# Kernel tuning notes

Hardware: AMD Instinct MI355X
Metric: run time of the kernel (lower is better)

Reference implementation:

```python
import jax, jax.numpy as jnp
import numpy as np

B, S, D = 1, 4096, 2048
M = 4                  # compression rate
NC = S // M            # compressed slots
TOPK = 512
NH, C = 16, 64         # query heads, head dim
DC = 512               # query compression dim
NG, DG = 4, 512        # output projection groups, intermediate dim
CI, NHI = 64, 4        # indexer head dim, indexer heads
ROPE = 32              # partial rope dims (last ROPE of C)
EPS = 1e-6
NEG = -1e30


def _ln(x, w, b):
    mu = x.mean(-1, keepdims=True)
    var = ((x - mu) ** 2).mean(-1, keepdims=True)
    return (x - mu) * jax.lax.rsqrt(var + EPS) * w + b


def _rope(q, pos):
    # partial RoPE on the last ROPE dims of q [B,S,NH,C]; keys are NOT rotated (faithful)
    x_part, x_rope = q[..., :C - ROPE], q[..., C - ROPE:]
    x0, x1 = x_rope[..., 0::2], x_rope[..., 1::2]
    inv = 1.0 / (10000.0 ** (jnp.arange(0, ROPE, 2, dtype=jnp.float32) / ROPE))
    ang = pos[:, None].astype(jnp.float32) * inv[None]           # [S, ROPE/2]
    cos = jnp.cos(ang)[None, :, None, :]
    sin = jnp.sin(ang)[None, :, None, :]
    r = x0 * cos - x1 * sin
    i = x0 * sin + x1 * cos
    rot = jnp.stack([r, i], -1).reshape(x_rope.shape)
    return jnp.concatenate([x_part, rot], -1)


def reference(x, w_kv_a, w_kv_b, w_z_a, w_z_b, b_a, b_b, w_dq, w_iuq, w_w, w_k,
              w_uq, o_down, o_up, kvn_w, kvn_b, qn_w, qn_b, sink_logits):
    pos = jnp.arange(S)
    # ---- token-level compressor: windowed (2m-wide, m-stride) per-channel softmax ----
    c_a = (x @ w_kv_a).reshape(B, NC, M, C)
    c_b = (x @ w_kv_b).reshape(B, NC, M, C)
    z_a = (x @ w_z_a).reshape(B, NC, M, C)
    z_b = (x @ w_z_b).reshape(B, NC, M, C)
    prev_z = jnp.concatenate([jnp.full((B, 1, M, C), NEG, x.dtype), z_b[:, :-1]], 1)
    prev_c = jnp.concatenate([jnp.zeros((B, 1, M, C), x.dtype), c_b[:, :-1]], 1)
    logits = jnp.concatenate([prev_z + b_b, z_a + b_a], 2)        # [B,NC,2M,C]
    wts = jax.nn.softmax(logits, axis=2)
    compressed = (wts * jnp.concatenate([prev_c, c_a], 2)).sum(2)  # [B,NC,C]
    # ---- lightning indexer: relu multi-head scores + causal mask + top-k ----
    c_q = x @ w_dq                                                 # [B,S,DC]
    q_i = (c_q @ w_iuq).reshape(B, S, NHI, CI)
    hw = x @ w_w                                                   # [B,S,NHI]
    k_orig = x.reshape(B, NC, M, D).mean(2)
    k_proj = k_orig @ w_k                                          # [B,NC,CI]
    dot = jnp.einsum('bshc,bkc->bskh', q_i, k_proj)
    iscores = (jax.nn.relu(dot) * hw[:, :, None, :]).sum(-1)       # [B,S,NC]
    imask = jnp.arange(NC)[None, None, :] < pos[None, :, None]     # NC//S + 1 == 1
    iscores = jnp.where(imask, iscores, -jnp.inf)
    _, top_idx = jax.lax.top_k(iscores, TOPK)                      # [B,S,K]
    # ---- sparse attention over gathered compressed KV ----
    q = (c_q @ w_uq).reshape(B, S, NH, C)
    kc = _ln(compressed, kvn_w, kvn_b)
    q = _rope(_ln(q, qn_w, qn_b), pos)
    k_sel = kc[jnp.arange(B)[:, None, None], top_idx]              # [B,S,K,C]
    scores = jnp.einsum('bshc,bskc->bhsk', q, k_sel) / jnp.sqrt(jnp.float32(C))
    cmask = pos[None, None, :, None] < (top_idx[:, None, :, :] * M)
    scores = jnp.where(cmask, scores, -jnp.inf)
    e = jnp.exp(scores)
    denom = e.sum(-1, keepdims=True) + jnp.exp(sink_logits)[None, :, None, None]
    attn = e / denom                                               # sink-augmented softmax
    out = jnp.einsum('bhsk,bskc->bshc', attn, k_sel).reshape(B, S, NH * C)
    g = jnp.einsum('bsgd,gde->bsge', out.reshape(B, S, NG, (NH * C) // NG), o_down)
    return g.reshape(B, S, NG * DG) @ o_up


def setup_inputs() -> dict:
    key = jax.random.key(0)
    ks = jax.random.split(key, 20)
    lin = lambda k, fi, fo: jax.random.normal(k, (fi, fo), jnp.float32) / np.sqrt(fi)
    return {
        'x': jax.random.normal(ks[0], (B, S, D), jnp.float32),
        'w_kv_a': lin(ks[1], D, C), 'w_kv_b': lin(ks[2], D, C),
        'w_z_a': lin(ks[3], D, C), 'w_z_b': lin(ks[4], D, C),
        'b_a': 0.02 * jax.random.normal(ks[5], (M, C), jnp.float32),
        'b_b': 0.02 * jax.random.normal(ks[6], (M, C), jnp.float32),
        'w_dq': lin(ks[7], D, DC),
        'w_iuq': lin(ks[8], DC, CI * NHI),
        'w_w': lin(ks[9], D, NHI),
        'w_k': lin(ks[10], D, CI),
        'w_uq': lin(ks[11], DC, NH * C),
        'o_down': jax.random.normal(ks[12], (NG, (NH * C) // NG, DG), jnp.float32) / np.sqrt((NH * C) // NG),
        'o_up': lin(ks[13], NG * DG, D),
        'kvn_w': 1.0 + 0.02 * jax.random.normal(ks[14], (C,), jnp.float32),
        'kvn_b': 0.02 * jax.random.normal(ks[15], (C,), jnp.float32),
        'qn_w': 1.0 + 0.02 * jax.random.normal(ks[16], (C,), jnp.float32),
        'qn_b': 0.02 * jax.random.normal(ks[17], (C,), jnp.float32),
        'sink_logits': 0.02 * jax.random.normal(ks[18], (NH,), jnp.float32),
    }
```

## Files before the change

kernel.cpp:

```cpp
#include <hip/hip_runtime.h>
#include <math.h>

#define S_   4096
#define D_   2048
#define M_   4
#define NC_  1024
#define TOPK_ 512
#define NH_  16
#define C_   64
#define DC_  512
#define NG_  4
#define DG_  512
#define CI_  64
#define NHI_ 4
#define ROPE_ 32
#define EPS_ 1e-6f

typedef __attribute__((ext_vector_type(8))) short short8;
typedef __attribute__((ext_vector_type(4))) short short4v;
typedef __attribute__((ext_vector_type(4))) float floatx4;

__device__ inline unsigned short f2bf(float f) {
  unsigned u = __float_as_uint(f);
  u += 0x7fff + ((u >> 16) & 1);
  return (unsigned short)(u >> 16);
}
__device__ inline float bf2f(unsigned short h) {
  return __uint_as_float(((unsigned)h) << 16);
}

__global__ __launch_bounds__(256) void gemm_bf16_64(
    const unsigned short* __restrict__ A, const unsigned short* __restrict__ Bt,
    float* __restrict__ Cf, unsigned short* __restrict__ Cb,
    int K, int lda, int ldb, int ldc,
    long long Az, long long Bz, long long Cz) {
  int zz = blockIdx.z;
  A += (size_t)zz * Az;
  Bt += (size_t)zz * Bz;
  if (Cf) Cf += (size_t)zz * Cz;
  if (Cb) Cb += (size_t)zz * Cz;
  __shared__ unsigned short As[64 * 32];
  __shared__ unsigned short Bs[128 * 32];
  int tid = threadIdx.x;
  int bm = blockIdx.y * 64, bn = blockIdx.x * 128;
  int lane = tid & 63, wid = tid >> 6;
  int wm = (wid & 1) * 32, wn = (wid >> 1) * 64;
  int qd = lane >> 4, m16 = lane & 15;

  floatx4 acc[2][4];
#pragma unroll
  for (int i = 0; i < 2; ++i)
#pragma unroll
    for (int j = 0; j < 4; ++j) acc[i][j] = (floatx4){0.f, 0.f, 0.f, 0.f};

  for (int k0 = 0; k0 < K; k0 += 32) {
    {
      int r = tid >> 2, sl = tid & 3;
      int g = sl ^ ((r >> 1) & 3);
      __builtin_amdgcn_global_load_lds(
          (const __attribute__((address_space(1))) unsigned int*)(A + (size_t)(bm + r) * lda + k0 + g * 8),
          (__attribute__((address_space(3))) unsigned int*)(&As[tid * 8]), 16, 0, 0);
    }
#pragma unroll
    for (int i = 0; i < 2; ++i) {
      int idx = tid + 256 * i;
      int r = idx >> 2, sl = idx & 3;
      int g = sl ^ ((r >> 1) & 3);
      __builtin_amdgcn_global_load_lds(
          (const __attribute__((address_space(1))) unsigned int*)(Bt + (size_t)(bn + r) * ldb + k0 + g * 8),
          (__attribute__((address_space(3))) unsigned int*)(&Bs[idx * 8]), 16, 0, 0);
    }
    __syncthreads();
    short8 af[2], bfr[4];
#pragma unroll
    for (int mi = 0; mi < 2; ++mi) {
      int r = wm + mi * 16 + m16;
      int slot = qd ^ ((r >> 1) & 3);
      af[mi] = *(const short8*)&As[r * 32 + slot * 8];
    }
#pragma unroll
    for (int ni = 0; ni < 4; ++ni) {
      int r = wn + ni * 16 + m16;
      int slot = qd ^ ((r >> 1) & 3);
      bfr[ni] = *(const short8*)&Bs[r * 32 + slot * 8];
    }
#pragma unroll
    for (int mi = 0; mi < 2; ++mi)
#pragma unroll
      for (int ni = 0; ni < 4; ++ni)
        acc[mi][ni] = __builtin_amdgcn_mfma_f32_16x16x32_bf16(af[mi], bfr[ni], acc[mi][ni], 0, 0, 0);
    __syncthreads();
  }
#pragma unroll
  for (int mi = 0; mi < 2; ++mi)
#pragma unroll
    for (int ni = 0; ni < 4; ++ni) {
      int col = bn + wn + ni * 16 + m16;
#pragma unroll
      for (int rg = 0; rg < 4; ++rg) {
        int row = bm + wm + mi * 16 + qd * 4 + rg;
        if (Cb)
          Cb[(size_t)row * ldc + col] = f2bf(acc[mi][ni][rg]);
        else
          Cf[(size_t)row * ldc + col] = acc[mi][ni][rg];
      }
    }
}

__global__ __launch_bounds__(256) void gemm_bf16_128(
    const unsigned short* __restrict__ A, const unsigned short* __restrict__ Bt,
    float* __restrict__ Cf, unsigned short* __restrict__ Cb,
    int K, int lda, int ldb, int ldc,
    long long Az, long long Bz, long long Cz) {
  int zz = blockIdx.z;
  A += (size_t)zz * Az;
  Bt += (size_t)zz * Bz;
  if (Cf) Cf += (size_t)zz * Cz;
  if (Cb) Cb += (size_t)zz * Cz;
  __shared__ unsigned short As[128 * 32];
  __shared__ unsigned short Bs[128 * 32];
  int tid = threadIdx.x;
  int bm = blockIdx.y * 128, bn = blockIdx.x * 128;
  int lane = tid & 63, wid = tid >> 6;
  int wm = (wid & 1) * 64, wn = (wid >> 1) * 64;
  int qd = lane >> 4, m16 = lane & 15;

  floatx4 acc[4][4];
#pragma unroll
  for (int i = 0; i < 4; ++i)
#pragma unroll
    for (int j = 0; j < 4; ++j) acc[i][j] = (floatx4){0.f, 0.f, 0.f, 0.f};

  for (int k0 = 0; k0 < K; k0 += 32) {
#pragma unroll
    for (int i = 0; i < 2; ++i) {
      int idx = tid + 256 * i;
      int r = idx >> 2, sl = idx & 3;
      int g = sl ^ ((r >> 1) & 3);
      __builtin_amdgcn_global_load_lds(
          (const __attribute__((address_space(1))) unsigned int*)(A + (size_t)(bm + r) * lda + k0 + g * 8),
          (__attribute__((address_space(3))) unsigned int*)(&As[idx * 8]), 16, 0, 0);
      __builtin_amdgcn_global_load_lds(
          (const __attribute__((address_space(1))) unsigned int*)(Bt + (size_t)(bn + r) * ldb + k0 + g * 8),
          (__attribute__((address_space(3))) unsigned int*)(&Bs[idx * 8]), 16, 0, 0);
    }
    __syncthreads();
    short8 af[4], bfr[4];
#pragma unroll
    for (int mi = 0; mi < 4; ++mi) {
      int r = wm + mi * 16 + m16;
      int slot = qd ^ ((r >> 1) & 3);
      af[mi] = *(const short8*)&As[r * 32 + slot * 8];
    }
#pragma unroll
    for (int ni = 0; ni < 4; ++ni) {
      int r = wn + ni * 16 + m16;
      int slot = qd ^ ((r >> 1) & 3);
      bfr[ni] = *(const short8*)&Bs[r * 32 + slot * 8];
    }
#pragma unroll
    for (int mi = 0; mi < 4; ++mi)
#pragma unroll
      for (int ni = 0; ni < 4; ++ni)
        acc[mi][ni] = __builtin_amdgcn_mfma_f32_16x16x32_bf16(af[mi], bfr[ni], acc[mi][ni], 0, 0, 0);
    __syncthreads();
  }
#pragma unroll
  for (int mi = 0; mi < 4; ++mi)
#pragma unroll
    for (int ni = 0; ni < 4; ++ni) {
      int col = bn + wn + ni * 16 + m16;
#pragma unroll
      for (int rg = 0; rg < 4; ++rg) {
        int row = bm + wm + mi * 16 + qd * 4 + rg;
        if (Cb)
          Cb[(size_t)row * ldc + col] = f2bf(acc[mi][ni][rg]);
        else
          Cf[(size_t)row * ldc + col] = acc[mi][ni][rg];
      }
    }
}

__global__ __launch_bounds__(256) void gemm_bf16_split_64(
    const unsigned short* __restrict__ Ah, const unsigned short* __restrict__ Al,
    const unsigned short* __restrict__ Bh, const unsigned short* __restrict__ Bl,
    float* __restrict__ Cf, int K, int lda, int ldb, int ldc,
    long long Az, long long Bz, long long Cz) {
  int zz = blockIdx.z;
  Ah += (size_t)zz * Az; Al += (size_t)zz * Az;
  Bh += (size_t)zz * Bz; Bl += (size_t)zz * Bz;
  Cf += (size_t)zz * Cz;
  __shared__ unsigned short Ash[64 * 32];
  __shared__ unsigned short Asl[64 * 32];
  __shared__ unsigned short Bsh[128 * 32];
  __shared__ unsigned short Bsl[128 * 32];
  int tid = threadIdx.x;
  int bm = blockIdx.y * 64, bn = blockIdx.x * 128;
  int lane = tid & 63, wid = tid >> 6;
  int wm = (wid & 1) * 32, wn = (wid >> 1) * 64;
  int qd = lane >> 4, m16 = lane & 15;

  floatx4 acc[2][4];
#pragma unroll
  for (int i = 0; i < 2; ++i)
#pragma unroll
    for (int j = 0; j < 4; ++j) acc[i][j] = (floatx4){0.f, 0.f, 0.f, 0.f};

  for (int k0 = 0; k0 < K; k0 += 32) {
    {
      int r = tid >> 2, sl = tid & 3;
      int g = sl ^ ((r >> 1) & 3);
      size_t aoff = (size_t)(bm + r) * lda + k0 + g * 8;
      __builtin_amdgcn_global_load_lds(
          (const __attribute__((address_space(1))) unsigned int*)(Ah + aoff),
          (__attribute__((address_space(3))) unsigned int*)(&Ash[tid * 8]), 16, 0, 0);
      __builtin_amdgcn_global_load_lds(
          (const __attribute__((address_space(1))) unsigned int*)(Al + aoff),
          (__attribute__((address_space(3))) unsigned int*)(&Asl[tid * 8]), 16, 0, 0);
    }
#pragma unroll
    for (int i = 0; i < 2; ++i) {
      int idx = tid + 256 * i;
      int r = idx >> 2, sl = idx & 3;
      int g = sl ^ ((r >> 1) & 3);
      size_t boff = (size_t)(bn + r) * ldb + k0 + g * 8;
      __builtin_amdgcn_global_load_lds(
          (const __attribute__((address_space(1))) unsigned int*)(Bh + boff),
          (__attribute__((address_space(3))) unsigned int*)(&Bsh[idx * 8]), 16, 0, 0);
      __builtin_amdgcn_global_load_lds(
          (const __attribute__((address_space(1))) unsigned int*)(Bl + boff),
          (__attribute__((address_space(3))) unsigned int*)(&Bsl[idx * 8]), 16, 0, 0);
    }
    __syncthreads();
    short8 afh[2], afl[2], bfh[4], bfl[4];
#pragma unroll
    for (int mi = 0; mi < 2; ++mi) {
      int r = wm + mi * 16 + m16;
      int slot = qd ^ ((r >> 1) & 3);
      afh[mi] = *(const short8*)&Ash[r * 32 + slot * 8];
      afl[mi] = *(const short8*)&Asl[r * 32 + slot * 8];
    }
#pragma unroll
    for (int ni = 0; ni < 4; ++ni) {
      int r = wn + ni * 16 + m16;
      int slot = qd ^ ((r >> 1) & 3);
      bfh[ni] = *(const short8*)&Bsh[r * 32 + slot * 8];
      bfl[ni] = *(const short8*)&Bsl[r * 32 + slot * 8];
    }
#pragma unroll
    for (int mi = 0; mi < 2; ++mi)
#pragma unroll
      for (int ni = 0; ni < 4; ++ni) {
        acc[mi][ni] = __builtin_amdgcn_mfma_f32_16x16x32_bf16(afh[mi], bfh[ni], acc[mi][ni], 0, 0, 0);
        acc[mi][ni] = __builtin_amdgcn_mfma_f32_16x16x32_bf16(afh[mi], bfl[ni], acc[mi][ni], 0, 0, 0);
        acc[mi][ni] = __builtin_amdgcn_mfma_f32_16x16x32_bf16(afl[mi], bfh[ni], acc[mi][ni], 0, 0, 0);
      }
    __syncthreads();
  }
#pragma unroll
  for (int mi = 0; mi < 2; ++mi)
#pragma unroll
    for (int ni = 0; ni < 4; ++ni) {
      int col = bn + wn + ni * 16 + m16;
#pragma unroll
      for (int rg = 0; rg < 4; ++rg) {
        int row = bm + wm + mi * 16 + qd * 4 + rg;
        Cf[(size_t)row * ldc + col] = acc[mi][ni][rg];
      }
    }
}

__global__ __launch_bounds__(256) void gemm_bf16_split_128(
    const unsigned short* __restrict__ Ah, const unsigned short* __restrict__ Al,
    const unsigned short* __restrict__ Bh, const unsigned short* __restrict__ Bl,
    float* __restrict__ Cf, int K, int lda, int ldb, int ldc,
    long long Az, long long Bz, long long Cz) {
  int zz = blockIdx.z;
  Ah += (size_t)zz * Az; Al += (size_t)zz * Az;
  Bh += (size_t)zz * Bz; Bl += (size_t)zz * Bz;
  Cf += (size_t)zz * Cz;
  __shared__ unsigned short Ash[128 * 32];
  __shared__ unsigned short Asl[128 * 32];
  __shared__ unsigned short Bsh[128 * 32];
  __shared__ unsigned short Bsl[128 * 32];
  int tid = threadIdx.x;
  int bm = blockIdx.y * 128, bn = blockIdx.x * 128;
  int lane = tid & 63, wid = tid >> 6;
  int wm = (wid & 1) * 64, wn = (wid >> 1) * 64;
  int qd = lane >> 4, m16 = lane & 15;

  floatx4 acc[4][4];
#pragma unroll
  for (int i = 0; i < 4; ++i)
#pragma unroll
    for (int j = 0; j < 4; ++j) acc[i][j] = (floatx4){0.f, 0.f, 0.f, 0.f};

  for (int k0 = 0; k0 < K; k0 += 32) {
#pragma unroll
    for (int i = 0; i < 2; ++i) {
      int idx = tid + 256 * i;
      int r = idx >> 2, sl = idx & 3;
      int g = sl ^ ((r >> 1) & 3);
      size_t aoff = (size_t)(bm + r) * lda + k0 + g * 8;
      size_t boff = (size_t)(bn + r) * ldb + k0 + g * 8;
      __builtin_amdgcn_global_load_lds(
          (const __attribute__((address_space(1))) unsigned int*)(Ah + aoff),
          (__attribute__((address_space(3))) unsigned int*)(&Ash[idx * 8]), 16, 0, 0);
      __builtin_amdgcn_global_load_lds(
          (const __attribute__((address_space(1))) unsigned int*)(Al + aoff),
          (__attribute__((address_space(3))) unsigned int*)(&Asl[idx * 8]), 16, 0, 0);
      __builtin_amdgcn_global_load_lds(
          (const __attribute__((address_space(1))) unsigned int*)(Bh + boff),
          (__attribute__((address_space(3))) unsigned int*)(&Bsh[idx * 8]), 16, 0, 0);
      __builtin_amdgcn_global_load_lds(
          (const __attribute__((address_space(1))) unsigned int*)(Bl + boff),
          (__attribute__((address_space(3))) unsigned int*)(&Bsl[idx * 8]), 16, 0, 0);
    }
    __syncthreads();
    short8 afh[4], afl[4], bfh[4], bfl[4];
#pragma unroll
    for (int mi = 0; mi < 4; ++mi) {
      int r = wm + mi * 16 + m16;
      int slot = qd ^ ((r >> 1) & 3);
      afh[mi] = *(const short8*)&Ash[r * 32 + slot * 8];
      afl[mi] = *(const short8*)&Asl[r * 32 + slot * 8];
    }
#pragma unroll
    for (int ni = 0; ni < 4; ++ni) {
      int r = wn + ni * 16 + m16;
      int slot = qd ^ ((r >> 1) & 3);
      bfh[ni] = *(const short8*)&Bsh[r * 32 + slot * 8];
      bfl[ni] = *(const short8*)&Bsl[r * 32 + slot * 8];
    }
#pragma unroll
    for (int mi = 0; mi < 4; ++mi)
#pragma unroll
      for (int ni = 0; ni < 4; ++ni) {
        acc[mi][ni] = __builtin_amdgcn_mfma_f32_16x16x32_bf16(afh[mi], bfh[ni], acc[mi][ni], 0, 0, 0);
        acc[mi][ni] = __builtin_amdgcn_mfma_f32_16x16x32_bf16(afh[mi], bfl[ni], acc[mi][ni], 0, 0, 0);
        acc[mi][ni] = __builtin_amdgcn_mfma_f32_16x16x32_bf16(afl[mi], bfh[ni], acc[mi][ni], 0, 0, 0);
      }
    __syncthreads();
  }
#pragma unroll
  for (int mi = 0; mi < 4; ++mi)
#pragma unroll
    for (int ni = 0; ni < 4; ++ni) {
      int col = bn + wn + ni * 16 + m16;
#pragma unroll
      for (int rg = 0; rg < 4; ++rg) {
        int row = bm + wm + mi * 16 + qd * 4 + rg;
        Cf[(size_t)row * ldc + col] = acc[mi][ni][rg];
      }
    }
}

__global__ void reduce_f32(const float* __restrict__ P, float* __restrict__ C, int n, int z) {
  int i = (blockIdx.x * 256 + threadIdx.x) * 4;
  if (i >= n) return;
  float4 a = *(const float4*)&P[i];
  for (int s = 1; s < z; ++s) {
    float4 b = *(const float4*)&P[(size_t)s * n + i];
    a.x += b.x; a.y += b.y; a.z += b.z; a.w += b.w;
  }
  *(float4*)&C[i] = a;
}

__global__ void reduce_cast_split(const float* __restrict__ P, unsigned short* __restrict__ hi,
                                  unsigned short* __restrict__ lo, int n, int z) {
  int i = (blockIdx.x * 256 + threadIdx.x) * 4;
  if (i >= n) return;
  float4 a = *(const float4*)&P[i];
  for (int s = 1; s < z; ++s) {
    float4 b = *(const float4*)&P[(size_t)s * n + i];
    a.x += b.x; a.y += b.y; a.z += b.z; a.w += b.w;
  }
  ushort4 h = make_ushort4(f2bf(a.x), f2bf(a.y), f2bf(a.z), f2bf(a.w));
  ushort4 l = make_ushort4(f2bf(a.x - bf2f(h.x)), f2bf(a.y - bf2f(h.y)),
                           f2bf(a.z - bf2f(h.z)), f2bf(a.w - bf2f(h.w)));
  *(ushort4*)&hi[i] = h;
  *(ushort4*)&lo[i] = l;
}

__global__ __launch_bounds__(256) void iscores_mfma(
    const unsigned short* __restrict__ Ah, const unsigned short* __restrict__ Al,
    const unsigned short* __restrict__ Bh, const unsigned short* __restrict__ Bl,
    const float* __restrict__ hw, float* __restrict__ isc) {
  int bm = blockIdx.y * 128, bn = blockIdx.x * 128;
  if (bn > (bm >> 2) + 30) return;
  __shared__ unsigned short Ash[128 * 32];
  __shared__ unsigned short Asl[128 * 32];
  __shared__ unsigned short Bsh[128 * 32];
  __shared__ unsigned short Bsl[128 * 32];
  int tid = threadIdx.x;
  int lane = tid & 63, wid = tid >> 6;
  int wm = (wid >> 1) * 64, wn = (wid & 1) * 64;
  int qd = lane >> 4, m16 = lane & 15;

  floatx4 acc[4][4];
#pragma unroll
  for (int i = 0; i < 4; ++i)
#pragma unroll
    for (int j = 0; j < 4; ++j) acc[i][j] = (floatx4){0.f, 0.f, 0.f, 0.f};

#pragma unroll
  for (int k0 = 0; k0 < 64; k0 += 32) {
#pragma unroll
    for (int i = 0; i < 2; ++i) {
      int idx = tid + 256 * i;
      int r = idx >> 2, s = idx & 3;
      int g = s ^ ((r >> 1) & 3);
      size_t aoff = (size_t)(bm + r) * 64 + k0 + g * 8;
      size_t boff = (size_t)(bn + r) * 64 + k0 + g * 8;
      __builtin_amdgcn_global_load_lds(
          (const __attribute__((address_space(1))) unsigned int*)(Ah + aoff),
          (__attribute__((address_space(3))) unsigned int*)(&Ash[idx * 8]), 16, 0, 0);
      __builtin_amdgcn_global_load_lds(
          (const __attribute__((address_space(1))) unsigned int*)(Al + aoff),
          (__attribute__((address_space(3))) unsigned int*)(&Asl[idx * 8]), 16, 0, 0);
      __builtin_amdgcn_global_load_lds(
          (const __attribute__((address_space(1))) unsigned int*)(Bh + boff),
          (__attribute__((address_space(3))) unsigned int*)(&Bsh[idx * 8]), 16, 0, 0);
      __builtin_amdgcn_global_load_lds(
          (const __attribute__((address_space(1))) unsigned int*)(Bl + boff),
          (__attribute__((address_space(3))) unsigned int*)(&Bsl[idx * 8]), 16, 0, 0);
    }
    __syncthreads();
    short8 afh[4], afl[4], bfh[4], bfl[4];
#pragma unroll
    for (int mi = 0; mi < 4; ++mi) {
      int r = wm + mi * 16 + m16;
      int slot = qd ^ ((r >> 1) & 3);
      afh[mi] = *(const short8*)&Ash[r * 32 + slot * 8];
      afl[mi] = *(const short8*)&Asl[r * 32 + slot * 8];
    }
#pragma unroll
    for (int ni = 0; ni < 4; ++ni) {
      int r = wn + ni * 16 + m16;
      int slot = qd ^ ((r >> 1) & 3);
      bfh[ni] = *(const short8*)&Bsh[r * 32 + slot * 8];
      bfl[ni] = *(const short8*)&Bsl[r * 32 + slot * 8];
    }
#pragma unroll
    for (int mi = 0; mi < 4; ++mi)
#pragma unroll
      for (int ni = 0; ni < 4; ++ni) {
        acc[mi][ni] = __builtin_amdgcn_mfma_f32_16x16x32_bf16(afh[mi], bfh[ni], acc[mi][ni], 0, 0, 0);
        acc[mi][ni] = __builtin_amdgcn_mfma_f32_16x16x32_bf16(afh[mi], bfl[ni], acc[mi][ni], 0, 0, 0);
        acc[mi][ni] = __builtin_amdgcn_mfma_f32_16x16x32_bf16(afl[mi], bfh[ni], acc[mi][ni], 0, 0, 0);
      }
    __syncthreads();
  }
#pragma unroll
  for (int mi = 0; mi < 4; ++mi) {
    int tok = ((bm + wm + mi * 16) >> 2) + qd;
    float4 hwv = *(const float4*)&hw[tok * 4];
#pragma unroll
    for (int ni = 0; ni < 4; ++ni) {
      floatx4 a = acc[mi][ni];
      float v = fmaxf(a[0], 0.f) * hwv.x + fmaxf(a[1], 0.f) * hwv.y +
                fmaxf(a[2], 0.f) * hwv.z + fmaxf(a[3], 0.f) * hwv.w;
      int col = bn + wn + ni * 16 + m16;
      isc[(size_t)tok * NC_ + col] = (col < tok) ? v : -__builtin_inff();
    }
  }
}

#define BM 64
#define BN 64
#define BK 16
#define KSL_ 16
#define KSLICE_ 128
__global__ __launch_bounds__(256) void gemm_f32_splitk(
    const float* __restrict__ A, const float* __restrict__ B,
    float* __restrict__ P, int lda, int ldb) {
  __shared__ float As[BK][BM + 4];
  __shared__ float Bs[BK][BN + 4];
  int tid = threadIdx.x;
  int bm = blockIdx.y * BM;
  int kbase = blockIdx.x * KSLICE_;
  int tr = tid >> 4;
  int tc = tid & 15;
  float acc[4][4] = {{0.f}};
  for (int k0 = kbase; k0 < kbase + KSLICE_; k0 += BK) {
    int ac = tid & 15;
    int ar0 = tid >> 4;
#pragma unroll
    for (int i = 0; i < 4; ++i) {
      int r = ar0 + 16 * i;
      As[ac][r] = A[(size_t)(bm + r) * lda + k0 + ac];
    }
    int bc = tid & 63;
    int br0 = tid >> 6;
#pragma unroll
    for (int i = 0; i < 4; ++i) {
      int r = br0 + 4 * i;
      Bs[r][bc] = B[(size_t)(k0 + r) * ldb + bc];
    }
    __syncthreads();
#pragma unroll
    for (int kk = 0; kk < BK; ++kk) {
      float4 av = *(const float4*)&As[kk][tr * 4];
      float4 bv = *(const float4*)&Bs[kk][tc * 4];
      float a[4] = {av.x, av.y, av.z, av.w};
      float b[4] = {bv.x, bv.y, bv.z, bv.w};
#pragma unroll
      for (int i = 0; i < 4; ++i)
#pragma unroll
        for (int j = 0; j < 4; ++j) acc[i][j] += a[i] * b[j];
    }
    __syncthreads();
  }
  float* Pb = P + (size_t)blockIdx.x * (NC_ * CI_);
#pragma unroll
  for (int i = 0; i < 4; ++i) {
    float4 v = make_float4(acc[i][0], acc[i][1], acc[i][2], acc[i][3]);
    *(float4*)&Pb[(size_t)(bm + tr * 4 + i) * CI_ + tc * 4] = v;
  }
}

__global__ void reduce_splitk(const float* __restrict__ P, float* __restrict__ C) {
  int i = blockIdx.x * 256 + threadIdx.x;
  if (i >= NC_ * CI_) return;
  float a = 0.f;
#pragma unroll
  for (int s = 0; s < KSL_; ++s) a += P[(size_t)s * (NC_ * CI_) + i];
  C[i] = a;
}

__global__ void cast_bf16(const float* __restrict__ in, unsigned short* __restrict__ out, int n) {
  int i = (blockIdx.x * 256 + threadIdx.x) * 4;
  if (i >= n) return;
  float4 v = *(const float4*)&in[i];
  ushort4 o = make_ushort4(f2bf(v.x), f2bf(v.y), f2bf(v.z), f2bf(v.w));
  *(ushort4*)&out[i] = o;
}

__global__ void cast_split(const float* __restrict__ in, unsigned short* __restrict__ hi,
                           unsigned short* __restrict__ lo, int n) {
  int i = (blockIdx.x * 256 + threadIdx.x) * 4;
  if (i >= n) return;
  float4 v = *(const float4*)&in[i];
  ushort4 h = make_ushort4(f2bf(v.x), f2bf(v.y), f2bf(v.z), f2bf(v.w));
  ushort4 l = make_ushort4(f2bf(v.x - bf2f(h.x)), f2bf(v.y - bf2f(h.y)),
                           f2bf(v.z - bf2f(h.z)), f2bf(v.w - bf2f(h.w)));
  *(ushort4*)&hi[i] = h;
  *(ushort4*)&lo[i] = l;
}

__device__ inline float wave_sum64(float v) {
#pragma unroll
  for (int off = 32; off > 0; off >>= 1) v += __shfl_xor(v, off, 64);
  return v;
}

__global__ __launch_bounds__(512) void cast_split_hw(
    const float* __restrict__ x, unsigned short* __restrict__ hi,
    unsigned short* __restrict__ lo, const float* __restrict__ ww,
    float* __restrict__ hw) {
  int s = blockIdx.x, tid = threadIdx.x;
  size_t i = (size_t)s * D_ + tid * 4;
  float4 v = *(const float4*)&x[i];
  ushort4 h = make_ushort4(f2bf(v.x), f2bf(v.y), f2bf(v.z), f2bf(v.w));
  ushort4 l = make_ushort4(f2bf(v.x - bf2f(h.x)), f2bf(v.y - bf2f(h.y)),
                           f2bf(v.z - bf2f(h.z)), f2bf(v.w - bf2f(h.w)));
  *(ushort4*)&hi[i] = h;
  *(ushort4*)&lo[i] = l;
  const float* wr = ww + tid * 16;
  float a0 = v.x * wr[0] + v.y * wr[4] + v.z * wr[8]  + v.w * wr[12];
  float a1 = v.x * wr[1] + v.y * wr[5] + v.z * wr[9]  + v.w * wr[13];
  float a2 = v.x * wr[2] + v.y * wr[6] + v.z * wr[10] + v.w * wr[14];
  float a3 = v.x * wr[3] + v.y * wr[7] + v.z * wr[11] + v.w * wr[15];
  a0 = wave_sum64(a0); a1 = wave_sum64(a1);
  a2 = wave_sum64(a2); a3 = wave_sum64(a3);
  __shared__ float red[8][4];
  int wid = tid >> 6, lane = tid & 63;
  if (lane == 0) { red[wid][0] = a0; red[wid][1] = a1; red[wid][2] = a2; red[wid][3] = a3; }
  __syncthreads();
  if (tid < 4) {
    float acc = 0.f;
#pragma unroll
    for (int w2 = 0; w2 < 8; ++w2) acc += red[w2][tid];
    hw[s * 4 + tid] = acc;
  }
}

__global__ __launch_bounds__(256) void transpose_cast(
    const float* __restrict__ in, unsigned short* __restrict__ out, int K, int N,
    long long inz, long long outz) {
  in += (size_t)blockIdx.z * inz;
  out += (size_t)blockIdx.z * outz;
  __shared__ float t[32][33];
  int k0 = blockIdx.x * 32, n0 = blockIdx.y * 32;
  int tx = threadIdx.x & 31, ty = threadIdx.x >> 5;
#pragma unroll
  for (int i = 0; i < 4; ++i)
    t[ty * 4 + i][tx] = in[(size_t)(k0 + ty * 4 + i) * N + n0 + tx];
  __syncthreads();
#pragma unroll
  for (int i = 0; i < 4; ++i)
    out[(size_t)(n0 + ty * 4 + i) * K + k0 + tx] = f2bf(t[tx][ty * 4 + i]);
}

__global__ __launch_bounds__(256) void transpose_cast_split(
    const float* __restrict__ in, unsigned short* __restrict__ outh,
    unsigned short* __restrict__ outl, int K, int N) {
  __shared__ float t[32][33];
  int k0 = blockIdx.x * 32, n0 = blockIdx.y * 32;
  int tx = threadIdx.x & 31, ty = threadIdx.x >> 5;
#pragma unroll
  for (int i = 0; i < 4; ++i)
    t[ty * 4 + i][tx] = in[(size_t)(k0 + ty * 4 + i) * N + n0 + tx];
  __syncthreads();
#pragma unroll
  for (int i = 0; i < 4; ++i) {
    float v = t[tx][ty * 4 + i];
    unsigned short h = f2bf(v);
    outh[(size_t)(n0 + ty * 4 + i) * K + k0 + tx] = h;
    outl[(size_t)(n0 + ty * 4 + i) * K + k0 + tx] = f2bf(v - bf2f(h));
  }
}

__global__ void mean4_kernel(const float* __restrict__ x, float* __restrict__ ko) {
  int i = blockIdx.x * 256 + threadIdx.x;
  if (i >= NC_ * D_) return;
  int j = i >> 11, d = i & (D_ - 1);
  const float* p = x + (size_t)j * 4 * D_ + d;
  ko[i] = 0.25f * (p[0] + p[D_] + p[2 * D_] + p[3 * D_]);
}

__global__ void gate_kernel(const float* __restrict__ c4,
                            const float* __restrict__ ba, const float* __restrict__ bb,
                            float* __restrict__ comp) {
  int i = blockIdx.x * 256 + threadIdx.x;
  if (i >= NC_ * C_) return;
  int j = i >> 6, c = i & 63;
  float lg[8], vv[8];
#pragma unroll
  for (int m = 0; m < 4; ++m) {
    if (j == 0) {
      lg[m] = -1e30f + bb[m * C_ + c];
      vv[m] = 0.f;
    } else {
      int row = (j - 1) * 4 + m;
      lg[m] = c4[(size_t)row * 256 + 192 + c] + bb[m * C_ + c];
      vv[m] = c4[(size_t)row * 256 + 64 + c];
    }
    int row2 = j * 4 + m;
    lg[4 + m] = c4[(size_t)row2 * 256 + 128 + c] + ba[m * C_ + c];
    vv[4 + m] = c4[(size_t)row2 * 256 + 0 + c];
  }
  float mx = lg[0];
#pragma unroll
  for (int t = 1; t < 8; ++t) mx = fmaxf(mx, lg[t]);
  float se = 0.f, acc = 0.f;
#pragma unroll
  for (int t = 0; t < 8; ++t) {
    float e = expf(lg[t] - mx);
    se += e;
    acc += e * vv[t];
  }
  comp[i] = acc / se;
}

__global__ void ln_kc_kernel(const float* __restrict__ in, const float* __restrict__ w,
                             const float* __restrict__ b, unsigned short* __restrict__ kcb,
                             unsigned short* __restrict__ kcbT) {
  int row = blockIdx.x * 4 + (threadIdx.x >> 6);
  int c = threadIdx.x & 63;
  float v = in[(size_t)row * C_ + c];
  float mu = wave_sum64(v) * (1.f / 64.f);
  float d = v - mu;
  float var = wave_sum64(d * d) * (1.f / 64.f);
  float y = d * (1.f / sqrtf(var + EPS_)) * w[c] + b[c];
  unsigned short h = f2bf(y);
  kcb[(size_t)row * C_ + c] = h;
  kcbT[(size_t)c * NC_ + row] = h;
}

__global__ void ln_rope_q_kernel(const float* __restrict__ quq, const float* __restrict__ w,
                                 const float* __restrict__ b, unsigned short* __restrict__ qb) {
  int row = blockIdx.x * 4 + (threadIdx.x >> 6);
  int s = row >> 4;
  int c = threadIdx.x & 63;
  float v = quq[(size_t)row * C_ + c];
  float mu = wave_sum64(v) * (1.f / 64.f);
  float d = v - mu;
  float var = wave_sum64(d * d) * (1.f / 64.f);
  float y = d * (1.f / sqrtf(var + EPS_)) * w[c] + b[c];
  float outv;
  float partner = __shfl_xor(y, 1, 64);
  if (c < C_ - ROPE_) {
    outv = y;
  } else {
    int p = (c - (C_ - ROPE_)) >> 1;
    float inv = powf(10000.f, -(2.f * (float)p) / (float)ROPE_);
    float ang = (float)s * inv;
    float cs = cosf(ang), sn = sinf(ang);
    if ((c & 1) == 0)
      outv = y * cs - partner * sn;
    else
      outv = partner * sn + y * cs;
  }
  qb[(size_t)row * C_ + c] = f2bf(outv * 0.125f);
}

#define MINF_ 0x007FFFFFu
__global__ __launch_bounds__(256) void topk_select_kernel(
    const float* __restrict__ isc, unsigned* __restrict__ sel) {
  __shared__ unsigned mv[NC_];
  __shared__ unsigned bins[256];
  __shared__ unsigned scan[256];
  __shared__ unsigned sB, sR;
  __shared__ unsigned selw[32];
  int s = blockIdx.x;
  int tid = threadIdx.x;
  for (int i = tid; i < NC_; i += 256) {
    if (i < s) {
      unsigned u = __float_as_uint(isc[(size_t)s * NC_ + i]);
      mv[i] = (u & 0x80000000u) ? ~u : (u | 0x80000000u);
    } else {
      mv[i] = MINF_;
    }
  }
  __syncthreads();
  unsigned K_rem = TOPK_;
  unsigned prefix = 0u;
  for (int lvl = 0; lvl < 4; ++lvl) {
// ... 288 lines not shown
```

Baseline: 436.8 us.

## Double-buffer LDS staging in bf16 GEMM kernels to overlap loads with MFMA

The bf16 GEMM kernels (64 and 128 tile) and the 128 split-precision GEMM now use two LDS buffers. The next K tile is issued via global_load_lds while MFMAs run on the current one, and one barrier per iteration replaces two. The bf16 kernels also widen the K step from 32 to 64 (two 32-slices per stage). The goal is to hide global-load latency, at the cost of more LDS per block, which may lower occupancy.

```diff
diff --git a/kernel.cpp b/kernel.cpp
--- a/kernel.cpp
+++ b/kernel.cpp
@@ -29,6 +29,10 @@
   return __uint_as_float(((unsigned)h) << 16);
 }
 
+#define GLD16(src, dst) __builtin_amdgcn_global_load_lds( \
+    (const __attribute__((address_space(1))) unsigned int*)(src), \
+    (__attribute__((address_space(3))) unsigned int*)(dst), 16, 0, 0)
+
 __global__ __launch_bounds__(256) void gemm_bf16_64(
     const unsigned short* __restrict__ A, const unsigned short* __restrict__ Bt,
     float* __restrict__ Cf, unsigned short* __restrict__ Cb,
@@ -39,8 +43,8 @@
   Bt += (size_t)zz * Bz;
   if (Cf) Cf += (size_t)zz * Cz;
   if (Cb) Cb += (size_t)zz * Cz;
-  __shared__ unsigned short As[64 * 32];
-  __shared__ unsigned short Bs[128 * 32];
+  __shared__ unsigned short As[2 * 2 * 64 * 32];
+  __shared__ unsigned short Bs[2 * 2 * 128 * 32];
   int tid = threadIdx.x;
   int bm = blockIdx.y * 64, bn = blockIdx.x * 128;
   int lane = tid & 63, wid = tid >> 6;
@@ -53,44 +57,62 @@
 #pragma unroll
     for (int j = 0; j < 4; ++j) acc[i][j] = (floatx4){0.f, 0.f, 0.f, 0.f};
 
-  for (int k0 = 0; k0 < K; k0 += 32) {
-    {
-      int r = tid >> 2, sl = tid & 3;
-      int g = sl ^ ((r >> 1) & 3);
-      __builtin_amdgcn_global_load_lds(
-          (const __attribute__((address_space(1))) unsigned int*)(A + (size_t)(bm + r) * lda + k0 + g * 8),
-          (__attribute__((address_space(3))) unsigned int*)(&As[tid * 8]), 16, 0, 0);
-    }
-#pragma unroll
-    for (int i = 0; i < 2; ++i) {
-      int idx = tid + 256 * i;
-      int r = idx >> 2, sl = idx & 3;
-      int g = sl ^ ((r >> 1) & 3);
-      __builtin_amdgcn_global_load_lds(
-          (const __attribute__((address_space(1))) unsigned int*)(Bt + (size_t)(bn + r) * ldb + k0 + g * 8),
-          (__attribute__((address_space(3))) unsigned int*)(&Bs[idx * 8]), 16, 0, 0);
-    }
-    __syncthreads();
-    short8 af[2], bfr[4];
-#pragma unroll
-    for (int mi = 0; mi < 2; ++mi) {
-      int r = wm + mi * 16 + m16;
-      int slot = qd ^ ((r >> 1) & 3);
-      af[mi] = *(const short8*)&As[r * 32 + slot * 8];
-    }
-#pragma unroll
-    for (int ni = 0; ni < 4; ++ni) {
-      int r = wn + ni * 16 + m16;
-      int slot = qd ^ ((r >> 1) & 3);
-      bfr[ni] = *(const short8*)&Bs[r * 32 + slot * 8];
-    }
-#pragma unroll
-    for (int mi = 0; mi < 2; ++mi)
-#pragma unroll
-      for (int ni = 0; ni < 4; ++ni)
-        acc[mi][ni] = __builtin_amdgcn_mfma_f32_16x16x32_bf16(af[mi], bfr[ni], acc[mi][ni], 0, 0, 0);
-    __syncthreads();
-  }
+  auto stage = [&](int buf, int kt) {
+#pragma unroll
+    for (int h = 0; h < 2; ++h) {
+      {
+        int rr = tid >> 2, ss = tid & 3;
+        int gg = ss ^ ((rr >> 1) & 3);
+        GLD16(A + (size_t)(bm + rr) * lda + kt + h * 32 + gg * 8,
+              &As[(buf * 2 + h) * 2048 + tid * 8]);
+      }
+#pragma unroll
+      for (int i = 0; i < 2; ++i) {
+        int idx = tid + 256 * i;
+        int rr = idx >> 2, ss = idx & 3;
+        int gg = ss ^ ((rr >> 1) & 3);
+        GLD16(Bt + (size_t)(bn + rr) * ldb + kt + h * 32 + gg * 8,
+              &Bs[(buf * 2 + h) * 4096 + idx * 8]);
+      }
+    }
+  };
+  auto compute = [&](int buf) {
+#pragma unroll
+    for (int h = 0; h < 2; ++h) {
+      const unsigned short* Ab = &As[(buf * 2 + h) * 2048];
+      const unsigned short* Bb = &Bs[(buf * 2 + h) * 4096];
+      short8 af[2], bfr[4];
+#pragma unroll
+      for (int mi = 0; mi < 2; ++mi) {
+        int r = wm + mi * 16 + m16;
+        int slot = qd ^ ((r >> 1) & 3);
+        af[mi] = *(const short8*)&Ab[r * 32 + slot * 8];
+      }
+#pragma unroll
+      for (int ni = 0; ni < 4; ++ni) {
+        int r = wn + ni * 16 + m16;
+        int slot = qd ^ ((r >> 1) & 3);
+        bfr[ni] = *(const short8*)&Bb[r * 32 + slot * 8];
+      }
+#pragma unroll
+      for (int mi = 0; mi < 2; ++mi)
+#pragma unroll
+        for (int ni = 0; ni < 4; ++ni)
+          acc[mi][ni] = __builtin_amdgcn_mfma_f32_16x16x32_bf16(af[mi], bfr[ni], acc[mi][ni], 0, 0, 0);
+    }
+  };
+
+  stage(0, 0);
+  __syncthreads();
+  int cur = 0;
+  for (int kt = 64; kt < K; kt += 64) {
+    stage(cur ^ 1, kt);
+    compute(cur);
+    __syncthreads();
+    cur ^= 1;
+  }
+  compute(cur);
+
 #pragma unroll
   for (int mi = 0; mi < 2; ++mi)
 #pragma unroll
@@ -117,8 +139,8 @@
   Bt += (size_t)zz * Bz;
   if (Cf) Cf += (size_t)zz * Cz;
   if (Cb) Cb += (size_t)zz * Cz;
-  __shared__ unsigned short As[128 * 32];
-  __shared__ unsigned short Bs[128 * 32];
+  __shared__ unsigned short As[2 * 2 * 128 * 32];
+  __shared__ unsigned short Bs[2 * 2 * 128 * 32];
   int tid = threadIdx.x;
   int bm = blockIdx.y * 128, bn = blockIdx.x * 128;
   int lane = tid & 63, wid = tid >> 6;
@@ -131,40 +153,58 @@
 #pragma unroll
     for (int j = 0; j < 4; ++j) acc[i][j] = (floatx4){0.f, 0.f, 0.f, 0.f};
 
-  for (int k0 = 0; k0 < K; k0 += 32) {
-#pragma unroll
-    for (int i = 0; i < 2; ++i) {
-      int idx = tid + 256 * i;
-      int r = idx >> 2, sl = idx & 3;
-      int g = sl ^ ((r >> 1) & 3);
-      __builtin_amdgcn_global_load_lds(
-          (const __attribute__((address_space(1))) unsigned int*)(A + (size_t)(bm + r) * lda + k0 + g * 8),
-          (__attribute__((address_space(3))) unsigned int*)(&As[idx * 8]), 16, 0, 0);
-      __builtin_amdgcn_global_load_lds(
-          (const __attribute__((address_space(1))) unsigned int*)(Bt + (size_t)(bn + r) * ldb + k0 + g * 8),
-          (__attribute__((address_space(3))) unsigned int*)(&Bs[idx * 8]), 16, 0, 0);
-    }
-    __syncthreads();
-    short8 af[4], bfr[4];
-#pragma unroll
-    for (int mi = 0; mi < 4; ++mi) {
-      int r = wm + mi * 16 + m16;
-      int slot = qd ^ ((r >> 1) & 3);
-      af[mi] = *(const short8*)&As[r * 32 + slot * 8];
-    }
-#pragma unroll
-    for (int ni = 0; ni < 4; ++ni) {
-      int r = wn + ni * 16 + m16;
-      int slot = qd ^ ((r >> 1) & 3);
-      bfr[ni] = *(const short8*)&Bs[r * 32 + slot * 8];
-    }
-#pragma unroll
-    for (int mi = 0; mi < 4; ++mi)
-#pragma unroll
-      for (int ni = 0; ni < 4; ++ni)
-        acc[mi][ni] = __builtin_amdgcn_mfma_f32_16x16x32_bf16(af[mi], bfr[ni], acc[mi][ni], 0, 0, 0);
-    __syncthreads();
-  }
+  auto stage = [&](int buf, int kt) {
+#pragma unroll
+    for (int h = 0; h < 2; ++h) {
+#pragma unroll
+      for (int i = 0; i < 2; ++i) {
+        int idx = tid + 256 * i;
+        int rr = idx >> 2, ss = idx & 3;
+        int gg = ss ^ ((rr >> 1) & 3);
+        GLD16(A + (size_t)(bm + rr) * lda + kt + h * 32 + gg * 8,
+              &As[(buf * 2 + h) * 4096 + idx * 8]);
+        GLD16(Bt + (size_t)(bn + rr) * ldb + kt + h * 32 + gg * 8,
+              &Bs[(buf * 2 + h) * 4096 + idx * 8]);
+      }
+    }
+  };
+  auto compute = [&](int buf) {
+#pragma unroll
+    for (int h = 0; h < 2; ++h) {
+      const unsigned short* Ab = &As[(buf * 2 + h) * 4096];
+      const unsigned short* Bb = &Bs[(buf * 2 + h) * 4096];
+      short8 af[4], bfr[4];
+#pragma unroll
+      for (int mi = 0; mi < 4; ++mi) {
+        int r = wm + mi * 16 + m16;
+        int slot = qd ^ ((r >> 1) & 3);
+        af[mi] = *(const short8*)&Ab[r * 32 + slot * 8];
+      }
+#pragma unroll
+      for (int ni = 0; ni < 4; ++ni) {
+        int r = wn + ni * 16 + m16;
+        int slot = qd ^ ((r >> 1) & 3);
+        bfr[ni] = *(const short8*)&Bb[r * 32 + slot * 8];
+      }
+#pragma unroll
+      for (int mi = 0; mi < 4; ++mi)
+#pragma unroll
+        for (int ni = 0; ni < 4; ++ni)
+          acc[mi][ni] = __builtin_amdgcn_mfma_f32_16x16x32_bf16(af[mi], bfr[ni], acc[mi][ni], 0, 0, 0);
+    }
+  };
+
+  stage(0, 0);
+  __syncthreads();
+  int cur = 0;
+  for (int kt = 64; kt < K; kt += 64) {
+    stage(cur ^ 1, kt);
+    compute(cur);
+    __syncthreads();
+    cur ^= 1;
+  }
+  compute(cur);
+
 #pragma unroll
   for (int mi = 0; mi < 4; ++mi)
 #pragma unroll
@@ -211,12 +251,8 @@
       int r = tid >> 2, sl = tid & 3;
       int g = sl ^ ((r >> 1) & 3);
       size_t aoff = (size_t)(bm + r) * lda + k0 + g * 8;
-      __builtin_amdgcn_global_load_lds(
-          (const __attribute__((address_space(1))) unsigned int*)(Ah + aoff),
-          (__attribute__((address_space(3))) unsigned int*)(&Ash[tid * 8]), 16, 0, 0);
-      __builtin_amdgcn_global_load_lds(
-          (const __attribute__((address_space(1))) unsigned int*)(Al + aoff),
-          (__attribute__((address_space(3))) unsigned int*)(&Asl[tid * 8]), 16, 0, 0);
+      GLD16(Ah + aoff, &Ash[tid * 8]);
+      GLD16(Al + aoff, &Asl[tid * 8]);
     }
 #pragma unroll
     for (int i = 0; i < 2; ++i) {
@@ -224,12 +260,8 @@
       int r = idx >> 2, sl = idx & 3;
       int g = sl ^ ((r >> 1) & 3);
       size_t boff = (size_t)(bn + r) * ldb + k0 + g * 8;
-      __builtin_amdgcn_global_load_lds(
-          (const __attribute__((address_space(1))) unsigned int*)(Bh + boff),
-          (__attribute__((address_space(3))) unsigned int*)(&Bsh[idx * 8]), 16, 0, 0);
-      __builtin_amdgcn_global_load_lds(
-          (const __attribute__((address_space(1))) unsigned int*)(Bl + boff),
-          (__attribute__((address_space(3))) unsigned int*)(&Bsl[idx * 8]), 16, 0, 0);
+      GLD16(Bh + boff, &Bsh[idx * 8]);
+      GLD16(Bl + boff, &Bsl[idx * 8]);
     }
     __syncthreads();
     short8 afh[2], afl[2], bfh[4], bfl[4];
@@ -279,10 +311,10 @@
   Ah += (size_t)zz * Az; Al += (size_t)zz * Az;
   Bh += (size_t)zz * Bz; Bl += (size_t)zz * Bz;
   Cf += (size_t)zz * Cz;
-  __shared__ unsigned short Ash[128 * 32];
-  __shared__ unsigned short Asl[128 * 32];
-  __shared__ unsigned short Bsh[128 * 32];
-  __shared__ unsigned short Bsl[128 * 32];
+  __shared__ unsigned short Ash[2 * 128 * 32];
+  __shared__ unsigned short Asl[2 * 128 * 32];
+  __shared__ unsigned short Bsh[2 * 128 * 32];
+  __shared__ unsigned short Bsl[2 * 128 * 32];
   int tid = threadIdx.x;
   int bm = blockIdx.y * 128, bn = blockIdx.x * 128;
   int lane = tid & 63, wid = tid >> 6;
@@ -295,42 +327,39 @@
 #pragma unroll
     for (int j = 0; j < 4; ++j) acc[i][j] = (floatx4){0.f, 0.f, 0.f, 0.f};
 
-  for (int k0 = 0; k0 < K; k0 += 32) {
+  auto stage = [&](int buf, int kt) {
 #pragma unroll
     for (int i = 0; i < 2; ++i) {
       int idx = tid + 256 * i;
-      int r = idx >> 2, sl = idx & 3;
-      int g = sl ^ ((r >> 1) & 3);
-      size_t aoff = (size_t)(bm + r) * lda + k0 + g * 8;
-      size_t boff = (size_t)(bn + r) * ldb + k0 + g * 8;
-      __builtin_amdgcn_global_load_lds(
-          (const __attribute__((address_space(1))) unsigned int*)(Ah + aoff),
-          (__attribute__((address_space(3))) unsigned int*)(&Ash[idx * 8]), 16, 0, 0);
-      __builtin_amdgcn_global_load_lds(
-          (const __attribute__((address_space(1))) unsigned int*)(Al + aoff),
-          (__attribute__((address_space(3))) unsigned int*)(&Asl[idx * 8]), 16, 0, 0);
-      __builtin_amdgcn_global_load_lds(
-          (const __attribute__((address_space(1))) unsigned int*)(Bh + boff),
-          (__attribute__((address_space(3))) unsigned int*)(&Bsh[idx * 8]), 16, 0, 0);
-      __builtin_amdgcn_global_load_lds(
-          (const __attribute__((address_space(1))) unsigned int*)(Bl + boff),
-          (__attribute__((address_space(3))) unsigned int*)(&Bsl[idx * 8]), 16, 0, 0);
-    }
-    __syncthreads();
+      int rr = idx >> 2, ss = idx & 3;
+      int gg = ss ^ ((rr >> 1) & 3);
+      size_t aoff = (size_t)(bm + rr) * lda + kt + gg * 8;
+      size_t boff = (size_t)(bn + rr) * ldb + kt + gg * 8;
+      GLD16(Ah + aoff, &Ash[buf * 4096 + idx * 8]);
+      GLD16(Al + aoff, &Asl[buf * 4096 + idx * 8]);
+      GLD16(Bh + boff, &Bsh[buf * 4096 + idx * 8]);
+      GLD16(Bl + boff, &Bsl[buf * 4096 + idx * 8]);
+    }
+  };
+  auto compute = [&](int buf) {
+    const unsigned short* Ahb = &Ash[buf * 4096];
+    const unsigned short* Alb = &Asl[buf * 4096];
+    const unsigned short* Bhb = &Bsh[buf * 4096];
+    const unsigned short* Blb = &Bsl[buf * 4096];
     short8 afh[4], afl[4], bfh[4], bfl[4];
 #pragma unroll
     for (int mi = 0; mi < 4; ++mi) {
       int r = wm + mi * 16 + m16;
       int slot = qd ^ ((r >> 1) & 3);
-      afh[mi] = *(const short8*)&Ash[r * 32 + slot * 8];
-      afl[mi] = *(const short8*)&Asl[r * 32 + slot * 8];
+      afh[mi] = *(const short8*)&Ahb[r * 32 + slot * 8];
+      afl[mi] = *(const short8*)&Alb[r * 32 + slot * 8];
     }
 #pragma unroll
     for (int ni = 0; ni < 4; ++ni) {
       int r = wn + ni * 16 + m16;
       int slot = qd ^ ((r >> 1) & 3);
-      bfh[ni] = *(const short8*)&Bsh[r * 32 + slot * 8];
-      bfl[ni] = *(const short8*)&Bsl[r * 32 + slot * 8];
+      bfh[ni] = *(const short8*)&Bhb[r * 32 + slot * 8];
+      bfl[ni] = *(const short8*)&Blb[r * 32 + slot * 8];
     }
 #pragma unroll
     for (int mi = 0; mi < 4; ++mi)
@@ -340,8 +369,19 @@
         acc[mi][ni] = __builtin_amdgcn_mfma_f32_16x16x32_bf16(afh[mi], bfl[ni], acc[mi][ni], 0, 0, 0);
         acc[mi][ni] = __builtin_amdgcn_mfma_f32_16x16x32_bf16(afl[mi], bfh[ni], acc[mi][ni], 0, 0, 0);
       }
-    __syncthreads();
-  }
+  };
+
+  stage(0, 0);
+  __syncthreads();
+  int cur = 0;
+  for (int kt = 32; kt < K; kt += 32) {
+    stage(cur ^ 1, kt);
+    compute(cur);
+    __syncthreads();
+    cur ^= 1;
+  }
+  compute(cur);
+
 #pragma unroll
   for (int mi = 0; mi < 4; ++mi)
 #pragma unroll
@@ -412,18 +452,10 @@
       int g = s ^ ((r >> 1) & 3);
       size_t aoff = (size_t)(bm + r) * 64 + k0 + g * 8;
       size_t boff = (size_t)(bn + r) * 64 + k0 + g * 8;
-      __builtin_amdgcn_global_load_lds(
-          (const __attribute__((address_space(1))) unsigned int*)(Ah + aoff),
-          (__attribute__((address_space(3))) unsigned int*)(&Ash[idx * 8]), 16, 0, 0);
-      __builtin_amdgcn_global_load_lds(
-          (const __attribute__((address_space(1))) unsigned int*)(Al + aoff),
-          (__attribute__((address_space(3))) unsigned int*)(&Asl[idx * 8]), 16, 0, 0);
-      __builtin_amdgcn_global_load_lds(
-          (const __attribute__((address_space(1))) unsigned int*)(Bh + boff),
-          (__attribute__((address_space(3))) unsigned int*)(&Bsh[idx * 8]), 16, 0, 0);
-      __builtin_amdgcn_global_load_lds(
-          (const __attribute__((address_space(1))) unsigned int*)(Bl + boff),
-          (__attribute__((address_space(3))) unsigned int*)(&Bsl[idx * 8]), 16, 0, 0);
+      GLD16(Ah + aoff, &Ash[idx * 8]);
+      GLD16(Al + aoff, &Asl[idx * 8]);
+      GLD16(Bh + boff, &Bsh[idx * 8]);
+      GLD16(Bl + boff, &Bsl[idx * 8]);
     }
     __syncthreads();
     short8 afh[4], afl[4], bfh[4], bfl[4];
```

Measured after the change: 433.8 us. Within noise of the previous version (-0.7%).
